# Kernel optimization log

Hardware: AMD Instinct MI355X
Metric: run time of the kernel (lower is better)

Reference implementation:

```python
import jax, jax.numpy as jnp
import numpy as np

K = 3  # hardcoded in TransitionUp.forward

def setup_inputs() -> dict:
    key = jax.random.key(0)
    ks = jax.random.split(key, 8)
    M, N = 32768, 8192
    UP_C, DOWN_C, OUT_C = 128, 256, 128
    return {
        "up_points": jax.random.normal(ks[0], (M, 3), dtype=jnp.float32),
        "up_features": jax.random.normal(ks[1], (M, UP_C), dtype=jnp.float32),
        "down_points": jax.random.normal(ks[2], (N, 3), dtype=jnp.float32),
        "down_features": jax.random.normal(ks[3], (N, DOWN_C), dtype=jnp.float32),
        # torch nn.Linear params: W [out,in], b [out]
        "W_up": jax.random.normal(ks[4], (OUT_C, UP_C), dtype=jnp.float32) / np.sqrt(UP_C),
        "b_up": jax.random.normal(ks[5], (OUT_C,), dtype=jnp.float32) * 0.01,
        "W_down": jax.random.normal(ks[6], (OUT_C, DOWN_C), dtype=jnp.float32) / np.sqrt(DOWN_C),
        "b_down": jax.random.normal(ks[7], (OUT_C,), dtype=jnp.float32) * 0.01,
    }

def interpolate_knn(query_points, dataset_points, dataset_features, k):
    # squared pairwise distances [M, N]
    delta = query_points[:, None, :] - dataset_points[None, :, :]
    dist = jnp.sum(delta * delta, axis=-1)
    neg_dist, knn_idx = jax.lax.top_k(-dist, k)  # smallest-k
    knn_dist = -neg_dist                           # [M, k]
    knn_feats = dataset_features[knn_idx]          # [M, k, C]
    recip = 1.0 / (knn_dist + 1e-8)
    weights = recip / jnp.sum(recip, axis=-1, keepdims=True)  # [M, k]
    return jnp.einsum('mk,mkc->mc', weights, knn_feats)

def reference(up_points, up_features, down_points, down_features, W_up, b_up, W_down, b_down):
    down_f = down_features @ W_down.T + b_down            # [N, OUT_C]
    interp_f = interpolate_knn(up_points, down_points, down_f, K)  # [M, OUT_C]
    return interp_f + (up_features @ W_up.T + b_up)
```

## Files before the change

### kernel.cpp

```cpp
#include <hip/hip_runtime.h>
#include <cfloat>

#define M_UP   32768
#define N_DOWN 8192
#define UPC    128
#define DOWNC  256
#define OUTC   128
#define NCHUNK 8
#define CHUNK  (N_DOWN / NCHUNK)
#define G      8
#define Q      2
#define PG     12

__device__ __forceinline__ void fma4(float4& acc, float s, const float4 w) {
    acc.x = fmaf(s, w.x, acc.x);
    acc.y = fmaf(s, w.y, acc.y);
    acc.z = fmaf(s, w.z, acc.z);
    acc.w = fmaf(s, w.w, acc.w);
}

__device__ __forceinline__ void top3_bl(float s, int idx,
                                        float& d0, float& d1, float& d2,
                                        int& i0, int& i1, int& i2) {
    bool c0 = s < d0, c1 = s < d1, c2 = s < d2;
    float n0 = fminf(d0, s);
    float n1 = __builtin_amdgcn_fmed3f(d0, d1, s);
    float n2 = __builtin_amdgcn_fmed3f(d1, d2, s);
    int m0 = c0 ? idx : i0;
    int m1 = c0 ? i0 : (c1 ? idx : i1);
    int m2 = c1 ? i1 : (c2 ? idx : i2);
    d0 = n0; d1 = n1; d2 = n2;
    i0 = m0; i1 = m1; i2 = m2;
}

__global__ __launch_bounds__(256) void transpose_w(
        const float* __restrict__ W_up, const float* __restrict__ W_down,
        float* __restrict__ wt_up, float* __restrict__ wt_down) {
    int e = blockIdx.x * 256 + threadIdx.x;
    if (e < DOWNC * OUTC) {
        int k = e >> 7, c = e & 127;
        wt_down[e] = W_down[c * DOWNC + k];
    } else {
        int e2 = e - DOWNC * OUTC;
        int k = e2 >> 7, c = e2 & 127;
        wt_up[e2] = W_up[c * UPC + k];
    }
}

template <int K>
__device__ __forceinline__ void gemm_tile32(
        const float* __restrict__ A, const float* __restrict__ WT,
        float* sA , float* sW ,
        int rbase, int tid, float4 acc[2][2]) {
    const int rl = tid & 15;
    const int c0 = (tid >> 4) * 8;
    #pragma unroll 1
    for (int ph = 0; ph < K / 32; ++ph) {
        if (ph) __syncthreads();
        {
            int r = tid >> 3, k4 = tid & 7;
            float4 v = *(const float4*)(A + (size_t)(rbase + r) * K + ph * 32 + k4 * 4);
            *(float4*)&sA[r * 36 + k4 * 4] = v;
        }
        #pragma unroll
        for (int i = 0; i < 4; ++i) {
            int idx = tid + i * 256;
            int kk = idx >> 5, cc = idx & 31;
            float4 v = *(const float4*)(WT + (size_t)(ph * 32 + kk) * OUTC + cc * 4);
            *(float4*)&sW[kk * OUTC + cc * 4] = v;
        }
        __syncthreads();
        #pragma unroll 4
        for (int kk = 0; kk < 32; ++kk) {
            float a0 = sA[rl * 36 + kk];
            float a1 = sA[(rl + 16) * 36 + kk];
            float4 w0 = *(const float4*)&sW[kk * OUTC + c0];
            float4 w1 = *(const float4*)&sW[kk * OUTC + c0 + 4];
            fma4(acc[0][0], a0, w0); fma4(acc[0][1], a0, w1);
            fma4(acc[1][0], a1, w0); fma4(acc[1][1], a1, w1);
        }
    }
}

__device__ __forceinline__ void down_body(
        const float* __restrict__ A, const float* __restrict__ WT,
        const float* __restrict__ bias, float* __restrict__ down_f,
        int rb, int tid, float* smem) {
    float* sA = smem;
    float* sW = smem + 1152;
    float4 acc[2][2] = {};
    gemm_tile32<DOWNC>(A, WT, sA, sW, rb * 32, tid, acc);
    const int rl = tid & 15;
    const int cg = (tid >> 4) * 2;
    const float4 b0 = ((const float4*)bias)[cg];
    const float4 b1 = ((const float4*)bias)[cg + 1];
    #pragma unroll
    for (int i = 0; i < 2; ++i) {
        const int row = rb * 32 + rl + 16 * i;
        float4 v0 = acc[i][0], v1 = acc[i][1];
        v0.x += b0.x; v0.y += b0.y; v0.z += b0.z; v0.w += b0.w;
        v1.x += b1.x; v1.y += b1.y; v1.z += b1.z; v1.w += b1.w;
        ((float4*)down_f)[row * 32 + cg] = v0;
        ((float4*)down_f)[row * 32 + cg + 1] = v1;
    }
}

__device__ __forceinline__ void knn_body(
        const float* __restrict__ up_points,
        const float* __restrict__ down_points,
        float2* __restrict__ part,
        int bx, int by, int tid, float* smem) {
    float* sx = smem;
    float* sy = smem + 1536;
    float* sz = smem + 3072;
    const int base = by * CHUNK;
    for (int t = tid; t < CHUNK; t += 256) {
        int g = base + t;
        int gi = t >> 3, j = t & 7;
        sx[PG * gi + j] = down_points[3 * g];
        sy[PG * gi + j] = down_points[3 * g + 1];
        sz[PG * gi + j] = down_points[3 * g + 2];
    }
    __syncthreads();

    const int m0 = bx * (256 * Q) + tid;
    const int m1 = m0 + 256;
    const float q0x = up_points[3 * m0];
    const float q0y = up_points[3 * m0 + 1];
    const float q0z = up_points[3 * m0 + 2];
    const float q1x = up_points[3 * m1];
    const float q1y = up_points[3 * m1 + 1];
    const float q1z = up_points[3 * m1 + 2];

    float a_gd0 = FLT_MAX, a_gd1 = FLT_MAX, a_gd2 = FLT_MAX;
    int   a_gi0 = 0, a_gi1 = 0, a_gi2 = 0;
    float b_gd0 = FLT_MAX, b_gd1 = FLT_MAX, b_gd2 = FLT_MAX;
    int   b_gi0 = 0, b_gi1 = 0, b_gi2 = 0;

    for (int gi = 0; gi < CHUNK / G; ++gi) {
        float4 x0 = *(const float4*)&sx[PG * gi], x1 = *(const float4*)&sx[PG * gi + 4];
        float4 y0 = *(const float4*)&sy[PG * gi], y1 = *(const float4*)&sy[PG * gi + 4];
        float4 z0 = *(const float4*)&sz[PG * gi], z1 = *(const float4*)&sz[PG * gi + 4];
        float px[G] = {x0.x, x0.y, x0.z, x0.w, x1.x, x1.y, x1.z, x1.w};
        float py[G] = {y0.x, y0.y, y0.z, y0.w, y1.x, y1.y, y1.z, y1.w};
        float pz[G] = {z0.x, z0.y, z0.z, z0.w, z1.x, z1.y, z1.z, z1.w};
        float s0[G], s1[G];
        #pragma unroll
        for (int j = 0; j < G; ++j) {
            float dx0 = q0x - px[j], dy0 = q0y - py[j], dz0 = q0z - pz[j];
            s0[j] = fmaf(dz0, dz0, fmaf(dy0, dy0, dx0 * dx0));
            float dx1 = q1x - px[j], dy1 = q1y - py[j], dz1 = q1z - pz[j];
            s1[j] = fmaf(dz1, dz1, fmaf(dy1, dy1, dx1 * dx1));
        }
        float gm0 = fminf(fminf(fminf(s0[0], s0[1]), fminf(s0[2], s0[3])),
                          fminf(fminf(s0[4], s0[5]), fminf(s0[6], s0[7])));
        float gm1 = fminf(fminf(fminf(s1[0], s1[1]), fminf(s1[2], s1[3])),
                          fminf(fminf(s1[4], s1[5]), fminf(s1[6], s1[7])));
        top3_bl(gm0, gi, a_gd0, a_gd1, a_gd2, a_gi0, a_gi1, a_gi2);
        top3_bl(gm1, gi, b_gd0, b_gd1, b_gd2, b_gi0, b_gi1, b_gi2);
    }

    #pragma unroll
    for (int qq = 0; qq < Q; ++qq) {
        const float qx = qq ? q1x : q0x;
        const float qy = qq ? q1y : q0y;
        const float qz = qq ? q1z : q0z;
        int bases[3];
        if (qq == 0) { bases[0] = a_gi0; bases[1] = a_gi1; bases[2] = a_gi2; }
        else         { bases[0] = b_gi0; bases[1] = b_gi1; bases[2] = b_gi2; }
        float D0 = FLT_MAX, D1 = FLT_MAX, D2 = FLT_MAX;
        int I0 = 0, I1 = 0, I2 = 0;
        #pragma unroll
        for (int t = 0; t < 3; ++t) {
            const int gb = bases[t];
            float4 x0 = *(const float4*)&sx[PG * gb], x1 = *(const float4*)&sx[PG * gb + 4];
            float4 y0 = *(const float4*)&sy[PG * gb], y1 = *(const float4*)&sy[PG * gb + 4];
            float4 z0 = *(const float4*)&sz[PG * gb], z1 = *(const float4*)&sz[PG * gb + 4];
            float px[G] = {x0.x, x0.y, x0.z, x0.w, x1.x, x1.y, x1.z, x1.w};
            float py[G] = {y0.x, y0.y, y0.z, y0.w, y1.x, y1.y, y1.z, y1.w};
            float pz[G] = {z0.x, z0.y, z0.z, z0.w, z1.x, z1.y, z1.z, z1.w};
            #pragma unroll
            for (int j = 0; j < G; ++j) {
                float dx = qx - px[j], dy = qy - py[j], dz = qz - pz[j];
                float s = fmaf(dz, dz, fmaf(dy, dy, dx * dx));
                top3_bl(s, base + gb * G + j, D0, D1, D2, I0, I1, I2);
            }
        }
        const int m = qq ? m1 : m0;
        const int o = (by * M_UP + m) * 3;
        part[o]     = make_float2(D0, __int_as_float(I0));
        part[o + 1] = make_float2(D1, __int_as_float(I1));
        part[o + 2] = make_float2(D2, __int_as_float(I2));
    }
}

__global__ __launch_bounds__(256) void fused_dp_knn(
        const float* __restrict__ down_features, const float* __restrict__ wt_down,
        const float* __restrict__ b_down, float* __restrict__ down_f,
        const float* __restrict__ up_points, const float* __restrict__ down_points,
        float2* __restrict__ part) {
    __shared__ __align__(16) float smem[5248];
    const int bid = blockIdx.x;
    if (bid < 512) {
        knn_body(up_points, down_points, part, bid & 63, bid >> 6,
                 threadIdx.x, smem);
    } else {
        down_body(down_features, wt_down, b_down, down_f, bid - 512,
                  threadIdx.x, smem);
    }
}

__global__ __launch_bounds__(256) void up_fused(
        const float* __restrict__ A, const float* __restrict__ WT,
        const float* __restrict__ bias, const float* __restrict__ down_f,
        const float2* __restrict__ part,
        float* __restrict__ out) {
    __shared__ __align__(16) float sAT[32][72];
    __shared__ __align__(16) float sW[32][128];
    const int tid = threadIdx.x;
    const int rt4 = (tid >> 4) * 4;
    const int ct  = tid & 15;
    const int rbase = blockIdx.x * 64;

    float4 acc[4][2] = {};
    #pragma unroll 1
    for (int ph = 0; ph < UPC / 32; ++ph) {
        if (ph) __syncthreads();
        {
            const int r = tid & 63, kq = tid >> 6;
            const float* Ar = A + (size_t)(rbase + r) * UPC + ph * 32 + kq * 8;
            float4 v0 = *(const float4*)Ar;
            float4 v1 = *(const float4*)(Ar + 4);
            const int k0 = kq * 8;
            sAT[k0 + 0][r] = v0.x; sAT[k0 + 1][r] = v0.y;
            sAT[k0 + 2][r] = v0.z; sAT[k0 + 3][r] = v0.w;
            sAT[k0 + 4][r] = v1.x; sAT[k0 + 5][r] = v1.y;
            sAT[k0 + 6][r] = v1.z; sAT[k0 + 7][r] = v1.w;
        }
        {
            const float4* Wp = (const float4*)(WT + (size_t)ph * 32 * OUTC);
            float4* sW4 = (float4*)&sW[0][0];
            #pragma unroll
            for (int i = 0; i < 4; ++i)
                sW4[tid + i * 256] = Wp[tid + i * 256];
        }
        __syncthreads();
        #pragma unroll 4
        for (int kk = 0; kk < 32; ++kk) {
            float4 a  = *(const float4*)&sAT[kk][rt4];
            float4 w0 = *(const float4*)&sW[kk][ct * 4];
            float4 w1 = *(const float4*)&sW[kk][64 + ct * 4];
            fma4(acc[0][0], a.x, w0); fma4(acc[0][1], a.x, w1);
            fma4(acc[1][0], a.y, w0); fma4(acc[1][1], a.y, w1);
            fma4(acc[2][0], a.z, w0); fma4(acc[2][1], a.z, w1);
            fma4(acc[3][0], a.w, w0); fma4(acc[3][1], a.w, w1);
        }
    }

    __syncthreads();
    float2* sP = (float2*)&sW[0][0];
    #pragma unroll
    for (int i = 0; i < 6; ++i) {
        int t = tid + i * 256;
        int s = t / 192;
        int o = t - s * 192;
        sP[t] = part[((size_t)s * M_UP + rbase) * 3 + o];
    }
    __syncthreads();

    const float4 b0 = ((const float4*)bias)[ct];
    const float4 b1 = ((const float4*)bias)[ct + 16];
    const float4* df4 = (const float4*)down_f;
    float4* out4 = (float4*)out;
    #pragma unroll
    for (int i = 0; i < 4; ++i) {
        const int lr = rt4 + i;
        const int m = rbase + lr;
        float D0 = FLT_MAX, D1 = FLT_MAX, D2 = FLT_MAX;
        int I0 = 0, I1 = 0, I2 = 0;
        #pragma unroll
        for (int s = 0; s < NCHUNK; ++s) {
            float2 v0 = sP[s * 192 + lr * 3];
            float2 v1 = sP[s * 192 + lr * 3 + 1];
            float2 v2 = sP[s * 192 + lr * 3 + 2];
            top3_bl(v0.x, __float_as_int(v0.y), D0, D1, D2, I0, I1, I2);
            top3_bl(v1.x, __float_as_int(v1.y), D0, D1, D2, I0, I1, I2);
            top3_bl(v2.x, __float_as_int(v2.y), D0, D1, D2, I0, I1, I2);
        }
        float r0 = 1.f / (D0 + 1e-8f);
        float r1 = 1.f / (D1 + 1e-8f);
        float r2 = 1.f / (D2 + 1e-8f);
        float rs = (r0 + r1) + r2;
        float w0 = r0 / rs, w1 = r1 / rs, w2 = r2 / rs;
        float4 f00 = df4[I0 * 32 + ct], f01 = df4[I0 * 32 + ct + 16];
        float4 f10 = df4[I1 * 32 + ct], f11 = df4[I1 * 32 + ct + 16];
        float4 f20 = df4[I2 * 32 + ct], f21 = df4[I2 * 32 + ct + 16];
        float4 res0, res1;
        res0.x = acc[i][0].x + b0.x + fmaf(w0, f00.x, fmaf(w1, f10.x, w2 * f20.x));
        res0.y = acc[i][0].y + b0.y + fmaf(w0, f00.y, fmaf(w1, f10.y, w2 * f20.y));
        res0.z = acc[i][0].z + b0.z + fmaf(w0, f00.z, fmaf(w1, f10.z, w2 * f20.z));
        res0.w = acc[i][0].w + b0.w + fmaf(w0, f00.w, fmaf(w1, f10.w, w2 * f20.w));
        res1.x = acc[i][1].x + b1.x + fmaf(w0, f01.x, fmaf(w1, f11.x, w2 * f21.x));
        res1.y = acc[i][1].y + b1.y + fmaf(w0, f01.y, fmaf(w1, f11.y, w2 * f21.y));
        res1.z = acc[i][1].z + b1.z + fmaf(w0, f01.z, fmaf(w1, f11.z, w2 * f21.z));
        res1.w = acc[i][1].w + b1.w + fmaf(w0, f01.w, fmaf(w1, f11.w, w2 * f21.w));
        out4[m * 32 + ct] = res0;
        out4[m * 32 + ct + 16] = res1;
    }
}

extern "C" void kernel_launch(void* const* d_in, const int* in_sizes, int n_in,
                              void* d_out, int out_size, void* d_ws, size_t ws_size,
                              hipStream_t stream) {
    const float* up_points     = (const float*)d_in[0];
    const float* up_features   = (const float*)d_in[1];
    const float* down_points   = (const float*)d_in[2];
    const float* down_features = (const float*)d_in[3];
    const float* W_up          = (const float*)d_in[4];
    const float* b_up          = (const float*)d_in[5];
    const float* W_down        = (const float*)d_in[6];
    const float* b_down        = (const float*)d_in[7];
    float* out = (float*)d_out;

    float* wt_down = (float*)d_ws;
    float* wt_up   = wt_down + DOWNC * OUTC;
    float* down_f  = wt_up + UPC * OUTC;
    float2* part   = (float2*)(down_f + N_DOWN * OUTC);

    transpose_w<<<(DOWNC * OUTC + UPC * OUTC) / 256, 256, 0, stream>>>(
        W_up, W_down, wt_up, wt_down);
    fused_dp_knn<<<768, 256, 0, stream>>>(
        down_features, wt_down, b_down, down_f, up_points, down_points, part);
    up_fused<<<M_UP / 64, 256, 0, stream>>>(
        up_features, wt_up, b_up, down_f, part, out);
}
```

Baseline: 164.6 us.

## Split KNN search into 16 dataset chunks and interleave down-GEMM blocks

Templates the KNN and merge kernels on the number of dataset chunks and, when the workspace is large enough, splits the dataset into 16 chunks instead of 8. That gives 1024 KNN blocks plus 256 down-projection blocks, interleaved one GEMM block after every four KNN blocks. The aim is more parallelism and better load balance across CUs. In exchange the partial top-3 buffer doubles, the merge kernel reads twice as many partial results, and it needs more shared memory for them.

After: 173.6 us. 5.5% more time.

```diff
diff --git a/kernel.cpp b/kernel.cpp
--- a/kernel.cpp
+++ b/kernel.cpp
@@ -6,8 +6,6 @@
 #define UPC    128
 #define DOWNC  256
 #define OUTC   128
-#define NCHUNK 8
-#define CHUNK  (N_DOWN / NCHUNK)
 #define G      8
 #define Q      2
 #define PG     12
@@ -105,16 +103,19 @@
     }
 }
 
-__device__ __forceinline__ void knn_body(
+template <int NC>
+__device__ __forceinline__ void knn_bodyT(
         const float* __restrict__ up_points,
         const float* __restrict__ down_points,
         float2* __restrict__ part,
         int bx, int by, int tid, float* smem) {
+    constexpr int CH = N_DOWN / NC;
+    constexpr int NG = CH / G;
     float* sx = smem;
-    float* sy = smem + 1536;
-    float* sz = smem + 3072;
-    const int base = by * CHUNK;
-    for (int t = tid; t < CHUNK; t += 256) {
+    float* sy = smem + PG * NG;
+    float* sz = smem + 2 * PG * NG;
+    const int base = by * CH;
+    for (int t = tid; t < CH; t += 256) {
         int g = base + t;
         int gi = t >> 3, j = t & 7;
         sx[PG * gi + j] = down_points[3 * g];
@@ -137,7 +138,7 @@
     float b_gd0 = FLT_MAX, b_gd1 = FLT_MAX, b_gd2 = FLT_MAX;
     int   b_gi0 = 0, b_gi1 = 0, b_gi2 = 0;
 
-    for (int gi = 0; gi < CHUNK / G; ++gi) {
+    for (int gi = 0; gi < NG; ++gi) {
         float4 x0 = *(const float4*)&sx[PG * gi], x1 = *(const float4*)&sx[PG * gi + 4];
         float4 y0 = *(const float4*)&sy[PG * gi], y1 = *(const float4*)&sy[PG * gi + 4];
         float4 z0 = *(const float4*)&sz[PG * gi], z1 = *(const float4*)&sz[PG * gi + 4];
@@ -171,8 +172,8 @@
         float D0 = FLT_MAX, D1 = FLT_MAX, D2 = FLT_MAX;
         int I0 = 0, I1 = 0, I2 = 0;
         #pragma unroll
-        for (int t = 0; t < 3; ++t) {
-            const int gb = bases[t];
+        for (int t3 = 0; t3 < 3; ++t3) {
+            const int gb = bases[t3];
             float4 x0 = *(const float4*)&sx[PG * gb], x1 = *(const float4*)&sx[PG * gb + 4];
             float4 y0 = *(const float4*)&sy[PG * gb], y1 = *(const float4*)&sy[PG * gb + 4];
             float4 z0 = *(const float4*)&sz[PG * gb], z1 = *(const float4*)&sz[PG * gb + 4];
@@ -194,6 +195,7 @@
     }
 }
 
+template <int NC>
 __global__ __launch_bounds__(256) void fused_dp_knn(
         const float* __restrict__ down_features, const float* __restrict__ wt_down,
         const float* __restrict__ b_down, float* __restrict__ down_f,
@@ -201,22 +203,36 @@
         float2* __restrict__ part) {
     __shared__ __align__(16) float smem[5248];
     const int bid = blockIdx.x;
-    if (bid < 512) {
-        knn_body(up_points, down_points, part, bid & 63, bid >> 6,
-                 threadIdx.x, smem);
+    if constexpr (NC == 8) {
+        if (bid < 512) {
+            knn_bodyT<8>(up_points, down_points, part, bid & 63, bid >> 6,
+                         threadIdx.x, smem);
+        } else {
+            down_body(down_features, wt_down, b_down, down_f, bid - 512,
+                      threadIdx.x, smem);
+        }
     } else {
-        down_body(down_features, wt_down, b_down, down_f, bid - 512,
-                  threadIdx.x, smem);
-    }
-}
-
+        const int grp = bid / 5, rid = bid % 5;
+        if (rid < 4) {
+            const int k = grp * 4 + rid;
+            knn_bodyT<16>(up_points, down_points, part, k & 63, k >> 6,
+                          threadIdx.x, smem);
+        } else {
+            down_body(down_features, wt_down, b_down, down_f, grp,
+                      threadIdx.x, smem);
+        }
+    }
+}
+
+template <int NC>
 __global__ __launch_bounds__(256) void up_fused(
         const float* __restrict__ A, const float* __restrict__ WT,
         const float* __restrict__ bias, const float* __restrict__ down_f,
         const float2* __restrict__ part,
         float* __restrict__ out) {
-    __shared__ __align__(16) float sAT[32][72];
-    __shared__ __align__(16) float sW[32][128];
+    __shared__ __align__(16) float usmem[6400];
+    float* sAT = usmem;
+    float* sW  = usmem + 2304;
     const int tid = threadIdx.x;
     const int rt4 = (tid >> 4) * 4;
     const int ct  = tid & 15;
@@ -232,14 +248,14 @@
             float4 v0 = *(const float4*)Ar;
             float4 v1 = *(const float4*)(Ar + 4);
             const int k0 = kq * 8;
-            sAT[k0 + 0][r] = v0.x; sAT[k0 + 1][r] = v0.y;
-            sAT[k0 + 2][r] = v0.z; sAT[k0 + 3][r] = v0.w;
-            sAT[k0 + 4][r] = v1.x; sAT[k0 + 5][r] = v1.y;
-            sAT[k0 + 6][r] = v1.z; sAT[k0 + 7][r] = v1.w;
+            sAT[(k0 + 0) * 72 + r] = v0.x; sAT[(k0 + 1) * 72 + r] = v0.y;
+            sAT[(k0 + 2) * 72 + r] = v0.z; sAT[(k0 + 3) * 72 + r] = v0.w;
+            sAT[(k0 + 4) * 72 + r] = v1.x; sAT[(k0 + 5) * 72 + r] = v1.y;
+            sAT[(k0 + 6) * 72 + r] = v1.z; sAT[(k0 + 7) * 72 + r] = v1.w;
         }
         {
             const float4* Wp = (const float4*)(WT + (size_t)ph * 32 * OUTC);
-            float4* sW4 = (float4*)&sW[0][0];
+            float4* sW4 = (float4*)sW;
             #pragma unroll
             for (int i = 0; i < 4; ++i)
                 sW4[tid + i * 256] = Wp[tid + i * 256];
@@ -247,9 +263,9 @@
         __syncthreads();
         #pragma unroll 4
         for (int kk = 0; kk < 32; ++kk) {
-            float4 a  = *(const float4*)&sAT[kk][rt4];
-            float4 w0 = *(const float4*)&sW[kk][ct * 4];
-            float4 w1 = *(const float4*)&sW[kk][64 + ct * 4];
+            float4 a  = *(const float4*)&sAT[kk * 72 + rt4];
+            float4 w0 = *(const float4*)&sW[kk * 128 + ct * 4];
+            float4 w1 = *(const float4*)&sW[kk * 128 + 64 + ct * 4];
             fma4(acc[0][0], a.x, w0); fma4(acc[0][1], a.x, w1);
             fma4(acc[1][0], a.y, w0); fma4(acc[1][1], a.y, w1);
             fma4(acc[2][0], a.z, w0); fma4(acc[2][1], a.z, w1);
@@ -258,9 +274,9 @@
     }
 
     __syncthreads();
-    float2* sP = (float2*)&sW[0][0];
+    float2* sP = (float2*)usmem;
     #pragma unroll
-    for (int i = 0; i < 6; ++i) {
+    for (int i = 0; i < NC * 192 / 256; ++i) {
         int t = tid + i * 256;
         int s = t / 192;
         int o = t - s * 192;
@@ -279,7 +295,7 @@
         float D0 = FLT_MAX, D1 = FLT_MAX, D2 = FLT_MAX;
         int I0 = 0, I1 = 0, I2 = 0;
         #pragma unroll
-        for (int s = 0; s < NCHUNK; ++s) {
+        for (int s = 0; s < NC; ++s) {
             float2 v0 = sP[s * 192 + lr * 3];
             float2 v1 = sP[s * 192 + lr * 3 + 1];
             float2 v2 = sP[s * 192 + lr * 3 + 2];
@@ -327,10 +343,22 @@
     float* down_f  = wt_up + UPC * OUTC;
     float2* part   = (float2*)(down_f + N_DOWN * OUTC);
 
+    const size_t base_bytes =
+        (size_t)(DOWNC * OUTC + UPC * OUTC + N_DOWN * OUTC) * sizeof(float);
+    const size_t need16 = base_bytes + (size_t)16 * M_UP * 3 * sizeof(float2);
+    const bool big = ws_size >= need16;
+
     transpose_w<<<(DOWNC * OUTC + UPC * OUTC) / 256, 256, 0, stream>>>(
         W_up, W_down, wt_up, wt_down);
-    fused_dp_knn<<<768, 256, 0, stream>>>(
-        down_features, wt_down, b_down, down_f, up_points, down_points, part);
-    up_fused<<<M_UP / 64, 256, 0, stream>>>(
-        up_features, wt_up, b_up, down_f, part, out);
-}
+    if (big) {
+        fused_dp_knn<16><<<1280, 256, 0, stream>>>(
+            down_features, wt_down, b_down, down_f, up_points, down_points, part);
+        up_fused<16><<<M_UP / 64, 256, 0, stream>>>(
+            up_features, wt_up, b_up, down_f, part, out);
+    } else {
+        fused_dp_knn<8><<<768, 256, 0, stream>>>(
+            down_features, wt_down, b_down, down_f, up_points, down_points, part);
+        up_fused<8><<<M_UP / 64, 256, 0, stream>>>(
+            up_features, wt_up, b_up, down_f, part, out);
+    }
+}
```
